# Performance work log

Hardware: AMD Instinct MI355X
Metric: run time of the kernel (lower is better)

## Reference

```python
import jax, jax.numpy as jnp
import numpy as np

WIN = (2, 6, 12)          # (win_Z, win_H, win_W)
HEADS = 6
DIM = 192
IMG = (8, 96, 180)        # (Z, H, W) after patch embedding
NWIN_TOK = WIN[0] * WIN[1] * WIN[2]            # 144 tokens per window
TYPE_W = (IMG[0] // WIN[0]) * (IMG[1] // WIN[1])  # num_Z*num_H = 64
BIAS_ROWS = (2 * WIN[2] - 1) * WIN[1] ** 2 * WIN[0] ** 2  # 3312


def _build_position_index(win):
    wZ, wH, wW = win
    czi = np.arange(wZ); czj = -np.arange(wZ) * wZ
    chi = np.arange(wH); chj = -np.arange(wH) * wH
    cw = np.arange(wW)
    c1 = np.stack(np.meshgrid(czi, chi, cw, indexing='ij'), 0).reshape(3, -1)
    c2 = np.stack(np.meshgrid(czj, chj, cw, indexing='ij'), 0).reshape(3, -1)
    coords = (c1[:, :, None] - c2[:, None, :]).transpose(1, 2, 0).copy()  # (N, N, 3)
    coords[:, :, 2] += wW - 1
    coords[:, :, 1] *= 2 * wW - 1
    coords[:, :, 0] *= (2 * wW - 1) * wH ** 2
    return jnp.asarray(coords.sum(-1).reshape(-1))  # (N*N,) int indices into bias table

POS_IDX = _build_position_index(WIN)


def _layernorm(x, g, b, eps=1e-5):
    m = jnp.mean(x, -1, keepdims=True)
    v = jnp.mean(jnp.square(x - m), -1, keepdims=True)
    return (x - m) * jax.lax.rsqrt(v + eps) * g + b


def setup_inputs() -> dict:
    key = jax.random.key(0)
    ks = jax.random.split(key, 8)
    Z, H, W = IMG
    x = jax.random.normal(ks[0], (1, Z * H * W, DIM), dtype=jnp.float32)
    std = 0.02
    return {
        'x': x,
        'w_qkv': jax.random.normal(ks[1], (DIM, 3 * DIM), dtype=jnp.float32) * std,
        'b_qkv': jnp.zeros((3 * DIM,), jnp.float32),
        'w_proj': jax.random.normal(ks[2], (DIM, DIM), dtype=jnp.float32) * std,
        'b_proj': jnp.zeros((DIM,), jnp.float32),
        'bias_table': jax.random.normal(ks[3], (BIAS_ROWS, TYPE_W, HEADS), dtype=jnp.float32) * std,
        'g1': jnp.ones((DIM,), jnp.float32), 'b1': jnp.zeros((DIM,), jnp.float32),
        'g2': jnp.ones((DIM,), jnp.float32), 'b2': jnp.zeros((DIM,), jnp.float32),
        'w_mlp': jax.random.normal(ks[4], (DIM, DIM), dtype=jnp.float32) * std,
        'b_mlp': jnp.zeros((DIM,), jnp.float32),
        'Z': Z, 'H': H, 'W': W, 'roll': 0,
    }


def reference(x, w_qkv, b_qkv, w_proj, b_proj, bias_table, g1, b1, g2, b2,
              w_mlp, b_mlp, Z, H, W, roll):
    # roll=0 path (is_rolling=False, mask=None), per init_kwargs
    B, T, C = x.shape
    wZ, wH, wW = WIN
    nZ, nH, nW = Z // wZ, H // wH, W // wW
    hd = C // HEADS
    scale = float(hd) ** 0.5
    N = NWIN_TOK

    shortcut = x
    # window partition: (B,Z,H,W,C) -> (B*nZ*nH*nW, N, C)
    xw = (x.reshape(B, nZ, wZ, nH, wH, nW, wW, C)
            .transpose(0, 1, 3, 5, 2, 4, 6, 7)
            .reshape(-1, N, C))
    Bw = xw.shape[0]

    qkv = (xw @ w_qkv + b_qkv).reshape(Bw, N, 3, HEADS, hd).transpose(2, 0, 3, 1, 4)
    q, k, v = qkv[0], qkv[1], qkv[2]                       # (Bw, heads, N, hd)

    attn = jnp.einsum('bhnd,bhmd->bhnm', q, k) / scale     # (Bw, heads, N, N)

    # earth-specific relative position bias: gather then broadcast over f = Bw // TYPE_W
    bias = bias_table[POS_IDX].reshape(N, N, TYPE_W, HEADS).transpose(2, 3, 0, 1)
    f = Bw // TYPE_W
    attn = (attn.reshape(f, TYPE_W, HEADS, N, N) + bias[None]).reshape(Bw, HEADS, N, N)

    attn = jax.nn.softmax(attn, axis=-1)
    out = jnp.einsum('bhnm,bhmd->bhnd', attn, v).transpose(0, 2, 1, 3).reshape(Bw, N, C)
    out = out @ w_proj + b_proj

    # window merge back to (B, Z*H*W, C)
    out = (out.reshape(B, nZ, nH, nW, wZ, wH, wW, C)
              .transpose(0, 1, 4, 2, 5, 3, 6, 7)
              .reshape(B, Z * H * W, C))

    x = shortcut + _layernorm(out, g1, b1)
    x = x + _layernorm(x @ w_mlp + b_mlp, g2, b2)
    return x
```

## Files before the change

kernel.cpp:

```cpp
#include <hip/hip_runtime.h>


typedef __attribute__((ext_vector_type(8))) short bfrag;
typedef __attribute__((ext_vector_type(4))) float f32x4;
typedef __attribute__((ext_vector_type(4))) unsigned short us4;
typedef __attribute__((ext_vector_type(8))) unsigned short us8;

__device__ __forceinline__ unsigned short f2bf(float f) {
    unsigned int u = __builtin_bit_cast(unsigned int, f);
    u += 0x7fffu + ((u >> 16) & 1u);
    return (unsigned short)(u >> 16);
}
__device__ __forceinline__ float bf2f(unsigned short s) {
    return __builtin_bit_cast(float, ((unsigned int)s) << 16);
}
__device__ __forceinline__ int token_of(int iw, int n) {
    int wi = iw % 15, hi = (iw / 15) % 16, zi = iw / 240;
    int ww = n % 12, hh = (n / 12) % 6, zz = n / 72;
    return ((zi * 2 + zz) * 96 + hi * 6 + hh) * 180 + wi * 12 + ww;
}

__global__ __launch_bounds__(256) void wconv(const float* __restrict__ w_qkv,
                                             unsigned short* __restrict__ wt) {
    int id = blockIdx.x * 256 + threadIdx.x;
    if (id >= 110592) return;
    int k = id / 576, c = id - k * 576;
    wt[c * 192 + k] = f2bf(w_qkv[id]);
}

__global__ __launch_bounds__(256) void xconv(const float* __restrict__ x,
                                             unsigned short* __restrict__ x_bf) {
    int id = blockIdx.x * 256 + threadIdx.x;
    if (id >= 3317760) return;
    const float* xp = x + (size_t)id * 8;
    float4 v0 = *(const float4*)xp;
    float4 v1 = *(const float4*)(xp + 4);
    us8 o;
    o[0] = f2bf(v0.x); o[1] = f2bf(v0.y); o[2] = f2bf(v0.z); o[3] = f2bf(v0.w);
    o[4] = f2bf(v1.x); o[5] = f2bf(v1.y); o[6] = f2bf(v1.z); o[7] = f2bf(v1.w);
    *(us8*)&x_bf[(size_t)id * 8] = o;
}

__global__ __launch_bounds__(256) void wconv2(const float* __restrict__ w_proj,
                                              const float* __restrict__ w_mlp,
                                              unsigned short* __restrict__ wp_t,
                                              unsigned short* __restrict__ wm_t) {
    int id = blockIdx.x * 256 + threadIdx.x;
    if (id >= 36864) return;
    const float* src = blockIdx.y ? w_mlp : w_proj;
    unsigned short* dst = blockIdx.y ? wm_t : wp_t;
    int n = id / 192, k = id - n * 192;
    dst[id] = f2bf(src[(size_t)k * 192 + n]);
}

__global__ __launch_bounds__(256) void bias_reorg(const float* __restrict__ bias_table,
                                                  unsigned short* __restrict__ bias_r) {
    __shared__ unsigned short T[384][68];
    int p0 = blockIdx.x * 64;
    int tid = threadIdx.x;
    for (int e = tid; e < 64 * 384; e += 256) {
        int pl = e / 384, th = e - pl * 384;
        int pair = p0 + pl;
        int i = pair / 144, j = pair - i * 144;
        int z1 = i / 72, h1 = (i / 12) % 6, w1 = i % 12;
        int z2 = j / 72, h2 = (j / 12) % 6, w2 = j % 12;
        int idx = (z1 + 2 * z2) * 828 + (h1 + 6 * h2) * 23 + (w1 - w2 + 11);
        T[th][pl] = f2bf(bias_table[(size_t)idx * 384 + th]);
    }
    __syncthreads();
    for (int e = tid; e < 384 * 16; e += 256) {
        int th = e >> 4, pc = e & 15;
        *(us4*)&bias_r[(size_t)th * 20736 + p0 + pc * 4] = *(const us4*)&T[th][pc * 4];
    }
}

__global__ __launch_bounds__(384) void qkattn(const unsigned short* __restrict__ x_bf,
                                              const unsigned short* __restrict__ wt,
                                              const float* __restrict__ b_qkv,
                                              const unsigned short* __restrict__ bias_r,
                                              unsigned short* __restrict__ o_ws) {
    __shared__ __align__(16) unsigned short Xw[144 * 200];
    __shared__ __align__(16) unsigned short Ql[2][144 * 40];
    __shared__ __align__(16) unsigned short Kl[2][144 * 40];
    __shared__ __align__(16) unsigned short Vt[2][32 * 168];
    int tid = threadIdx.x;
    int iw = blockIdx.x;
    int w = tid >> 6, l = tid & 63, li = l & 15, lg = l >> 4;
    int tri = w / 3, tw = w - tri * 3;

#pragma unroll
    for (int i = 0; i < 9; ++i) {
        int idx = tid + i * 384;
        int r = idx / 24, g = idx - r * 24;
        *(uint4*)&Xw[r * 200 + g * 8] =
            *(const uint4*)&x_bf[(size_t)token_of(iw, r) * 192 + g * 8];
    }
    __syncthreads();

    for (int rnd = 0; rnd < 3; ++rnd) {
        int h = rnd * 2 + tri;

        if (tw < 2) {
            int wrow = tw * 192 + h * 32;
            f32x4 acc[9][2];
#pragma unroll
            for (int tt = 0; tt < 9; ++tt)
#pragma unroll
                for (int ct = 0; ct < 2; ++ct) acc[tt][ct] = (f32x4){0.f, 0.f, 0.f, 0.f};
            for (int kk = 0; kk < 6; ++kk) {
                int k0 = kk * 32 + lg * 8;
                bfrag wf[2];
#pragma unroll
                for (int ct = 0; ct < 2; ++ct)
                    wf[ct] = *(const bfrag*)&wt[(size_t)(wrow + ct * 16 + li) * 192 + k0];
#pragma unroll
                for (int tt = 0; tt < 9; ++tt) {
                    bfrag xf = *(const bfrag*)&Xw[(tt * 16 + li) * 200 + k0];
                    acc[tt][0] = __builtin_amdgcn_mfma_f32_16x16x32_bf16(xf, wf[0], acc[tt][0], 0, 0, 0);
                    acc[tt][1] = __builtin_amdgcn_mfma_f32_16x16x32_bf16(xf, wf[1], acc[tt][1], 0, 0, 0);
                }
            }
            unsigned short* dst = (tw == 0) ? &Ql[tri][0] : &Kl[tri][0];
#pragma unroll
            for (int ct = 0; ct < 2; ++ct) {
                float bq = b_qkv[tw * 192 + h * 32 + ct * 16 + li];
#pragma unroll
                for (int tt = 0; tt < 9; ++tt)
#pragma unroll
                    for (int r = 0; r < 4; ++r)
                        dst[(tt * 16 + lg * 4 + r) * 40 + ct * 16 + li] = f2bf(acc[tt][ct][r] + bq);
            }
        } else {
            int wrow = 2 * 192 + h * 32;
            f32x4 acc[2][9];
#pragma unroll
            for (int ct = 0; ct < 2; ++ct)
#pragma unroll
                for (int tt = 0; tt < 9; ++tt) acc[ct][tt] = (f32x4){0.f, 0.f, 0.f, 0.f};
            for (int kk = 0; kk < 6; ++kk) {
                int k0 = kk * 32 + lg * 8;
                bfrag wf[2];
#pragma unroll
                for (int ct = 0; ct < 2; ++ct)
                    wf[ct] = *(const bfrag*)&wt[(size_t)(wrow + ct * 16 + li) * 192 + k0];
#pragma unroll
                for (int tt = 0; tt < 9; ++tt) {
                    bfrag xf = *(const bfrag*)&Xw[(tt * 16 + li) * 200 + k0];
                    acc[0][tt] = __builtin_amdgcn_mfma_f32_16x16x32_bf16(wf[0], xf, acc[0][tt], 0, 0, 0);
                    acc[1][tt] = __builtin_amdgcn_mfma_f32_16x16x32_bf16(wf[1], xf, acc[1][tt], 0, 0, 0);
                }
            }
#pragma unroll
            for (int ct = 0; ct < 2; ++ct) {
                float4 bq = *(const float4*)&b_qkv[2 * 192 + h * 32 + ct * 16 + lg * 4];
                float bqa[4] = {bq.x, bq.y, bq.z, bq.w};
#pragma unroll
                for (int tt = 0; tt < 9; ++tt)
#pragma unroll
                    for (int r = 0; r < 4; ++r)
                        Vt[tri][(ct * 16 + lg * 4 + r) * 168 + tt * 16 + li] = f2bf(acc[ct][tt][r] + bqa[r]);
            }
            int d = l >> 1, half = l & 1;
            *(uint4*)&Vt[tri][d * 168 + 144 + half * 8] = (uint4){0u, 0u, 0u, 0u};
        }
        __syncthreads();

        int it0 = tw * 3;
        unsigned short* Pbw = &Ql[tri][(size_t)tw * 48 * 40];
        bfrag qf[3];
#pragma unroll
        for (int itl = 0; itl < 3; ++itl)
            qf[itl] = *(const bfrag*)&Ql[tri][((it0 + itl) * 16 + li) * 40 + lg * 8];

        f32x4 S[9][3];
#pragma unroll
        for (int jt = 0; jt < 9; ++jt) {
            bfrag kf = *(const bfrag*)&Kl[tri][(jt * 16 + li) * 40 + lg * 8];
#pragma unroll
            for (int itl = 0; itl < 3; ++itl) {
                f32x4 z = (f32x4){0.f, 0.f, 0.f, 0.f};
                S[jt][itl] = __builtin_amdgcn_mfma_f32_16x16x32_bf16(kf, qf[itl], z, 0, 0, 0);
            }
        }

        const unsigned short* bp = bias_r + ((size_t)((iw & 63) * 6 + h)) * 20736;
        const float inv_scale = 0.17677669529663687f;
#pragma unroll
        for (int jt = 0; jt < 9; ++jt) {
#pragma unroll
            for (int itl = 0; itl < 3; ++itl) {
                int i = (it0 + itl) * 16 + li;
                int j0 = jt * 16 + lg * 4;
                us4 bv = *(const us4*)&bp[i * 144 + j0];
#pragma unroll
                for (int r = 0; r < 4; ++r)
                    S[jt][itl][r] = S[jt][itl][r] * inv_scale + bf2f(bv[r]);
            }
        }

        float inv[3];
#pragma unroll
        for (int itl = 0; itl < 3; ++itl) {
            float mx = -3.0e38f;
#pragma unroll
            for (int jt = 0; jt < 9; ++jt)
#pragma unroll
                for (int r = 0; r < 4; ++r) mx = fmaxf(mx, S[jt][itl][r]);
            mx = fmaxf(mx, __shfl_xor(mx, 16));
            mx = fmaxf(mx, __shfl_xor(mx, 32));
            float sum = 0.f;
#pragma unroll
            for (int jt = 0; jt < 9; ++jt)
#pragma unroll
                for (int r = 0; r < 4; ++r) {
                    float e = __expf(S[jt][itl][r] - mx);
                    S[jt][itl][r] = e;
                    sum += e;
                }
            sum += __shfl_xor(sum, 16);
            sum += __shfl_xor(sum, 32);
            inv[itl] = 1.f / sum;
        }

        f32x4 O[2][3];
#pragma unroll
        for (int dt = 0; dt < 2; ++dt)
#pragma unroll
            for (int itl = 0; itl < 3; ++itl) O[dt][itl] = (f32x4){0.f, 0.f, 0.f, 0.f};

        for (int jc = 0; jc < 5; ++jc) {
#pragma unroll
            for (int itl = 0; itl < 3; ++itl) {
                int irow = itl * 16 + li;
#pragma unroll
                for (int half = 0; half < 2; ++half) {
                    int jt = jc * 2 + half;
                    us4 pk;
                    if (jt < 9) {
                        pk[0] = f2bf(S[jt][itl][0]); pk[1] = f2bf(S[jt][itl][1]);
                        pk[2] = f2bf(S[jt][itl][2]); pk[3] = f2bf(S[jt][itl][3]);
                    } else {
                        pk = (us4){0, 0, 0, 0};
                    }
                    *(us4*)&Pbw[irow * 40 + half * 16 + lg * 4] = pk;
                }
            }
            bfrag pf[3], af[2];
#pragma unroll
            for (int itl = 0; itl < 3; ++itl)
                pf[itl] = *(const bfrag*)&Pbw[(itl * 16 + li) * 40 + lg * 8];
#pragma unroll
            for (int dt = 0; dt < 2; ++dt)
                af[dt] = *(const bfrag*)&Vt[tri][(dt * 16 + li) * 168 + jc * 32 + lg * 8];
#pragma unroll
            for (int dt = 0; dt < 2; ++dt)
#pragma unroll
                for (int itl = 0; itl < 3; ++itl)
                    O[dt][itl] = __builtin_amdgcn_mfma_f32_16x16x32_bf16(af[dt], pf[itl], O[dt][itl], 0, 0, 0);
        }

#pragma unroll
        for (int itl = 0; itl < 3; ++itl) {
#pragma unroll
            for (int dt = 0; dt < 2; ++dt) {
                us4 ov;
                ov[0] = f2bf(O[dt][itl][0] * inv[itl]);
                ov[1] = f2bf(O[dt][itl][1] * inv[itl]);
                ov[2] = f2bf(O[dt][itl][2] * inv[itl]);
                ov[3] = f2bf(O[dt][itl][3] * inv[itl]);
                *(us4*)&Pbw[(itl * 16 + li) * 40 + dt * 16 + lg * 4] = ov;
            }
        }
#pragma unroll
        for (int s = 0; s < 3; ++s) {
            int gi = s * 64 + l;
            int row = gi >> 2, g = gi & 3;
            uint4 v = *(const uint4*)&Pbw[row * 40 + g * 8];
            int t = token_of(iw, it0 * 16 + row);
            *(uint4*)&o_ws[(size_t)t * 192 + h * 32 + g * 8] = v;
        }
        __syncthreads();
    }
}

__global__ __launch_bounds__(512) void mlp_mfma(const unsigned short* __restrict__ o_ws,
                                                const float* __restrict__ x,
                                                const unsigned short* __restrict__ wp_t,
                                                const float* __restrict__ b_proj,
                                                const float* __restrict__ g1,
                                                const float* __restrict__ b1,
                                                const float* __restrict__ g2,
                                                const float* __restrict__ b2,
                                                const unsigned short* __restrict__ wm_t,
                                                const float* __restrict__ b_mlp,
                                                float* __restrict__ out) {
    __shared__ __align__(16) unsigned short Al[128 * 200];
    __shared__ __align__(16) unsigned short Bf[192 * 200];
    int tid = threadIdx.x;
    int t0 = blockIdx.x * 128;
    int w = tid >> 6, l = tid & 63, li = l & 15, lg = l >> 4;

#pragma unroll
    for (int i = 0; i < 9; ++i) {
        int idx = tid + i * 512;
        int r = idx / 24, g = idx - r * 24;
        *(uint4*)&Bf[r * 200 + g * 8] = *(const uint4*)&wp_t[(size_t)r * 192 + g * 8];
    }
    __syncthreads();

    f32x4 C[12];
#pragma unroll
    for (int nt = 0; nt < 12; ++nt) C[nt] = (f32x4){0.f, 0.f, 0.f, 0.f};
    for (int kk = 0; kk < 6; ++kk) {
        int k0 = kk * 32 + lg * 8;
        bfrag a = *(const bfrag*)&o_ws[(size_t)(t0 + w * 16 + li) * 192 + k0];
#pragma unroll
        for (int nt = 0; nt < 12; ++nt) {
            bfrag b = *(const bfrag*)&Bf[(nt * 16 + li) * 200 + k0];
            C[nt] = __builtin_amdgcn_mfma_f32_16x16x32_bf16(a, b, C[nt], 0, 0, 0);
        }
    }
    __syncthreads();

#pragma unroll
    for (int i = 0; i < 9; ++i) {
        int idx = tid + i * 512;
        int r = idx / 24, g = idx - r * 24;
        *(uint4*)&Bf[r * 200 + g * 8] = *(const uint4*)&wm_t[(size_t)r * 192 + g * 8];
    }

    {
        float bp[12], gg[12], bb[12];
#pragma unroll
        for (int nt = 0; nt < 12; ++nt) {
            int f = nt * 16 + li;
            bp[nt] = b_proj[f]; gg[nt] = g1[f]; bb[nt] = b1[f];
        }
#pragma unroll
        for (int r = 0; r < 4; ++r) {
            float s1 = 0.f;
#pragma unroll
            for (int nt = 0; nt < 12; ++nt) s1 += C[nt][r] + bp[nt];
            s1 += __shfl_xor(s1, 1); s1 += __shfl_xor(s1, 2);
            s1 += __shfl_xor(s1, 4); s1 += __shfl_xor(s1, 8);
            float mean = s1 * (1.f / 192.f);
            float s2 = 0.f;
#pragma unroll
            for (int nt = 0; nt < 12; ++nt) {
                float dv = C[nt][r] + bp[nt] - mean; s2 += dv * dv;
            }
            s2 += __shfl_xor(s2, 1); s2 += __shfl_xor(s2, 2);
            s2 += __shfl_xor(s2, 4); s2 += __shfl_xor(s2, 8);
            float rstd = rsqrtf(s2 * (1.f / 192.f) + 1e-5f);
            int row = w * 16 + lg * 4 + r;
            int t = t0 + row;
#pragma unroll
            for (int nt = 0; nt < 12; ++nt) {
                int f = nt * 16 + li;
                float ln = (C[nt][r] + bp[nt] - mean) * rstd * gg[nt] + bb[nt];
                float x1 = x[(size_t)t * 192 + f] + ln;
                C[nt][r] = x1;
                Al[row * 200 + f] = f2bf(x1);
            }
        }
    }
    __syncthreads();

    f32x4 C2[12];
#pragma unroll
    for (int nt = 0; nt < 12; ++nt) C2[nt] = (f32x4){0.f, 0.f, 0.f, 0.f};
    for (int kk = 0; kk < 6; ++kk) {
        int k0 = kk * 32 + lg * 8;
        bfrag a = *(const bfrag*)&Al[(w * 16 + li) * 200 + k0];
#pragma unroll
        for (int nt = 0; nt < 12; ++nt) {
            bfrag b = *(const bfrag*)&Bf[(nt * 16 + li) * 200 + k0];
            C2[nt] = __builtin_amdgcn_mfma_f32_16x16x32_bf16(a, b, C2[nt], 0, 0, 0);
        }
    }

    {
        float bp[12], gg[12], bb[12];
#pragma unroll
        for (int nt = 0; nt < 12; ++nt) {
            int f = nt * 16 + li;
            bp[nt] = b_mlp[f]; gg[nt] = g2[f]; bb[nt] = b2[f];
        }
#pragma unroll
        for (int r = 0; r < 4; ++r) {
            float s1 = 0.f;
#pragma unroll
            for (int nt = 0; nt < 12; ++nt) s1 += C2[nt][r] + bp[nt];
            s1 += __shfl_xor(s1, 1); s1 += __shfl_xor(s1, 2);
            s1 += __shfl_xor(s1, 4); s1 += __shfl_xor(s1, 8);
            float mean = s1 * (1.f / 192.f);
            float s2 = 0.f;
#pragma unroll
            for (int nt = 0; nt < 12; ++nt) {
                float dv = C2[nt][r] + bp[nt] - mean; s2 += dv * dv;
            }
            s2 += __shfl_xor(s2, 1); s2 += __shfl_xor(s2, 2);
            s2 += __shfl_xor(s2, 4); s2 += __shfl_xor(s2, 8);
            float rstd = rsqrtf(s2 * (1.f / 192.f) + 1e-5f);
            int t = t0 + w * 16 + lg * 4 + r;
#pragma unroll
            for (int nt = 0; nt < 12; ++nt) {
                int f = nt * 16 + li;
                float ln = (C2[nt][r] + bp[nt] - mean) * rstd * gg[nt] + bb[nt];
                out[(size_t)t * 192 + f] = C[nt][r] + ln;
            }
        }
    }
}

extern "C" void kernel_launch(void* const* d_in, const int* in_sizes, int n_in,
                              void* d_out, int out_size, void* d_ws, size_t ws_size,
                              hipStream_t stream) {
    const float* x          = (const float*)d_in[0];
    const float* w_qkv      = (const float*)d_in[1];
    const float* b_qkv      = (const float*)d_in[2];
    const float* w_proj     = (const float*)d_in[3];
    const float* b_proj     = (const float*)d_in[4];
    const float* bias_table = (const float*)d_in[5];
    const float* g1         = (const float*)d_in[6];
    const float* b1         = (const float*)d_in[7];
    const float* g2         = (const float*)d_in[8];
    const float* b2         = (const float*)d_in[9];
    const float* w_mlp      = (const float*)d_in[10];
    const float* b_mlp      = (const float*)d_in[11];

    char* ws = (char*)d_ws;
    unsigned short* bias_r = (unsigned short*)ws;
    unsigned short* o_ws   = (unsigned short*)(ws + 15925248);
    unsigned short* x_bf   = (unsigned short*)(ws + 69009408);
    unsigned short* w_t    = (unsigned short*)(ws + 122093568);
    unsigned short* wp_t   = (unsigned short*)(ws + 122314752);
    unsigned short* wm_t   = (unsigned short*)(ws + 122388480);

    wconv<<<432, 256, 0, stream>>>(w_qkv, w_t);
    xconv<<<12960, 256, 0, stream>>>(x, x_bf);
    bias_reorg<<<324, 256, 0, stream>>>(bias_table, bias_r);
    qkattn<<<960, 384, 0, stream>>>(x_bf, w_t, b_qkv, bias_r, o_ws);
    wconv2<<<dim3(144, 2), 256, 0, stream>>>(w_proj, w_mlp, wp_t, wm_t);
    mlp_mfma<<<1080, 512, 0, stream>>>(o_ws, x, wp_t, b_proj, g1, b1, g2, b2,
                                       wm_t, b_mlp, (float*)d_out);
}
```

Measured before the change: 280.9 us.

## Read window tokens directly from global memory in QKV projection, dropping LDS staging

Removes the shared-memory staging buffer for the window's input tokens, and each wave now loads its X fragments straight from global memory using precomputed token row offsets. The Q/K and V paths are unified to one transposed MFMA orientation, and Q/K outputs are written as packed 4-element vector stores. This frees about 57KB of LDS per block, which may allow more blocks per CU, and removes a barrier. In exchange it re-reads X from global or L2 memory six times per round across the waves and in every round, raising memory traffic.

```diff
diff --git a/kernel.cpp b/kernel.cpp
--- a/kernel.cpp
+++ b/kernel.cpp
@@ -79,7 +79,6 @@
                                               const float* __restrict__ b_qkv,
                                               const unsigned short* __restrict__ bias_r,
                                               unsigned short* __restrict__ o_ws) {
-    __shared__ __align__(16) unsigned short Xw[144 * 200];
     __shared__ __align__(16) unsigned short Ql[2][144 * 40];
     __shared__ __align__(16) unsigned short Kl[2][144 * 40];
     __shared__ __align__(16) unsigned short Vt[2][32 * 168];
@@ -88,68 +87,49 @@
     int w = tid >> 6, l = tid & 63, li = l & 15, lg = l >> 4;
     int tri = w / 3, tw = w - tri * 3;
 
-#pragma unroll
-    for (int i = 0; i < 9; ++i) {
-        int idx = tid + i * 384;
-        int r = idx / 24, g = idx - r * 24;
-        *(uint4*)&Xw[r * 200 + g * 8] =
-            *(const uint4*)&x_bf[(size_t)token_of(iw, r) * 192 + g * 8];
-    }
-    __syncthreads();
+    int xrow[9];
+#pragma unroll
+    for (int tt = 0; tt < 9; ++tt)
+        xrow[tt] = token_of(iw, tt * 16 + li) * 192;
 
     for (int rnd = 0; rnd < 3; ++rnd) {
         int h = rnd * 2 + tri;
 
+        int wrow = tw * 192 + h * 32;
+        f32x4 acc[2][9];
+#pragma unroll
+        for (int ct = 0; ct < 2; ++ct)
+#pragma unroll
+            for (int tt = 0; tt < 9; ++tt) acc[ct][tt] = (f32x4){0.f, 0.f, 0.f, 0.f};
+        for (int kk = 0; kk < 6; ++kk) {
+            int k0 = kk * 32 + lg * 8;
+            bfrag wf[2];
+#pragma unroll
+            for (int ct = 0; ct < 2; ++ct)
+                wf[ct] = *(const bfrag*)&wt[(size_t)(wrow + ct * 16 + li) * 192 + k0];
+#pragma unroll
+            for (int tt = 0; tt < 9; ++tt) {
+                bfrag xf = *(const bfrag*)&x_bf[(size_t)xrow[tt] + k0];
+                acc[0][tt] = __builtin_amdgcn_mfma_f32_16x16x32_bf16(wf[0], xf, acc[0][tt], 0, 0, 0);
+                acc[1][tt] = __builtin_amdgcn_mfma_f32_16x16x32_bf16(wf[1], xf, acc[1][tt], 0, 0, 0);
+            }
+        }
         if (tw < 2) {
-            int wrow = tw * 192 + h * 32;
-            f32x4 acc[9][2];
-#pragma unroll
-            for (int tt = 0; tt < 9; ++tt)
-#pragma unroll
-                for (int ct = 0; ct < 2; ++ct) acc[tt][ct] = (f32x4){0.f, 0.f, 0.f, 0.f};
-            for (int kk = 0; kk < 6; ++kk) {
-                int k0 = kk * 32 + lg * 8;
-                bfrag wf[2];
-#pragma unroll
-                for (int ct = 0; ct < 2; ++ct)
-                    wf[ct] = *(const bfrag*)&wt[(size_t)(wrow + ct * 16 + li) * 192 + k0];
+            unsigned short* dst = (tw == 0) ? &Ql[tri][0] : &Kl[tri][0];
+#pragma unroll
+            for (int ct = 0; ct < 2; ++ct) {
+                float4 bq = *(const float4*)&b_qkv[tw * 192 + h * 32 + ct * 16 + lg * 4];
 #pragma unroll
                 for (int tt = 0; tt < 9; ++tt) {
-                    bfrag xf = *(const bfrag*)&Xw[(tt * 16 + li) * 200 + k0];
-                    acc[tt][0] = __builtin_amdgcn_mfma_f32_16x16x32_bf16(xf, wf[0], acc[tt][0], 0, 0, 0);
-                    acc[tt][1] = __builtin_amdgcn_mfma_f32_16x16x32_bf16(xf, wf[1], acc[tt][1], 0, 0, 0);
+                    us4 o;
+                    o[0] = f2bf(acc[ct][tt][0] + bq.x);
+                    o[1] = f2bf(acc[ct][tt][1] + bq.y);
+                    o[2] = f2bf(acc[ct][tt][2] + bq.z);
+                    o[3] = f2bf(acc[ct][tt][3] + bq.w);
+                    *(us4*)&dst[(tt * 16 + li) * 40 + ct * 16 + lg * 4] = o;
                 }
             }
-            unsigned short* dst = (tw == 0) ? &Ql[tri][0] : &Kl[tri][0];
-#pragma unroll
-            for (int ct = 0; ct < 2; ++ct) {
-                float bq = b_qkv[tw * 192 + h * 32 + ct * 16 + li];
-#pragma unroll
-                for (int tt = 0; tt < 9; ++tt)
-#pragma unroll
-                    for (int r = 0; r < 4; ++r)
-                        dst[(tt * 16 + lg * 4 + r) * 40 + ct * 16 + li] = f2bf(acc[tt][ct][r] + bq);
-            }
         } else {
-            int wrow = 2 * 192 + h * 32;
-            f32x4 acc[2][9];
-#pragma unroll
-            for (int ct = 0; ct < 2; ++ct)
-#pragma unroll
-                for (int tt = 0; tt < 9; ++tt) acc[ct][tt] = (f32x4){0.f, 0.f, 0.f, 0.f};
-            for (int kk = 0; kk < 6; ++kk) {
-                int k0 = kk * 32 + lg * 8;
-                bfrag wf[2];
-#pragma unroll
-                for (int ct = 0; ct < 2; ++ct)
-                    wf[ct] = *(const bfrag*)&wt[(size_t)(wrow + ct * 16 + li) * 192 + k0];
-#pragma unroll
-                for (int tt = 0; tt < 9; ++tt) {
-                    bfrag xf = *(const bfrag*)&Xw[(tt * 16 + li) * 200 + k0];
-                    acc[0][tt] = __builtin_amdgcn_mfma_f32_16x16x32_bf16(wf[0], xf, acc[0][tt], 0, 0, 0);
-                    acc[1][tt] = __builtin_amdgcn_mfma_f32_16x16x32_bf16(wf[1], xf, acc[1][tt], 0, 0, 0);
-                }
-            }
 #pragma unroll
             for (int ct = 0; ct < 2; ++ct) {
                 float4 bq = *(const float4*)&b_qkv[2 * 192 + h * 32 + ct * 16 + lg * 4];
```

After: 497.7 us. +77.2%, slower.
